# Performance work log

Hardware: AMD Instinct MI355X
Metric: run time of the kernel (lower is better)

## Reference

```python
import jax, jax.numpy as jnp
import numpy as np

NEG_SLOPE = 0.01  # torch leaky_relu default

def _lrelu(x):
    return jax.nn.leaky_relu(x, NEG_SLOPE)

def _l2norm(x, axis):
    # torch F.normalize(p=2, eps=1e-12)
    n = jnp.linalg.norm(x, axis=axis, keepdims=True)
    return x / jnp.maximum(n, 1e-12)

def setup_inputs() -> dict:
    key = jax.random.key(0)
    ks = jax.random.split(key, 12)
    Nda, Nq, C, Din, Dout = 10000, 64, 1024, 128, 256
    target_adj = (jax.random.uniform(ks[0], (Nda, Nda)) < 0.002).astype(jnp.float32)
    query_adj = (jax.random.uniform(ks[1], (Nq, Nq)) < 0.2).astype(jnp.float32)
    node_features_da = jax.random.normal(ks[2], (Nda, Din), dtype=jnp.float32)
    node_features_q = jax.random.normal(ks[3], (Nq, Din), dtype=jnp.float32)
    candidate_set = jax.random.randint(ks[4], (C,), 0, Nda)
    candidate_adj = (jax.random.uniform(ks[5], (C, C)) < 0.01).astype(jnp.float32)
    s_in = 1.0 / np.sqrt(Din).astype(np.float32)
    s_out = 1.0 / np.sqrt(Dout).astype(np.float32)
    W1_da = jax.random.normal(ks[6], (Din, Dout), dtype=jnp.float32) * s_in
    W1_q = jax.random.normal(ks[7], (Din, Dout), dtype=jnp.float32) * s_in
    W2_da = jax.random.normal(ks[8], (Dout, Dout), dtype=jnp.float32) * s_out
    W2_q = jax.random.normal(ks[9], (Dout, Dout), dtype=jnp.float32) * s_out
    threshold = jnp.float32(0.2)
    return {"target_adj": target_adj, "node_features_da": node_features_da,
            "query_adj": query_adj, "node_features_q": node_features_q,
            "candidate_set": candidate_set, "candidate_adj": candidate_adj,
            "threshold": threshold, "W1_da": W1_da, "W1_q": W1_q,
            "W2_da": W2_da, "W2_q": W2_q}

def _cross_cosine(q, da, candidate_set):
    # cosine similarity between each query node and each candidate target node: [Nq, C]
    return _l2norm(q, 1) @ _l2norm(da[candidate_set], 1).T

def reference(target_adj, node_features_da, query_adj, node_features_q,
              candidate_set, candidate_adj, threshold, W1_da, W1_q, W2_da, W2_q):
    # layer 1: GCN propagation on both graphs (gcn(adj,x) = adj @ x @ W)
    da1 = _lrelu(target_adj @ (node_features_da @ W1_da))   # [Nda, D]
    q1 = _lrelu(query_adj @ (node_features_q @ W1_q))       # [Nq, D]
    c1 = _cross_cosine(q1, da1, candidate_set)               # [Nq, C]
    pre_da1 = da1[candidate_set]                             # [C, D]
    # NOTE: da1[candidate_set].data = ... mutates a temporary in torch -> no-op on da1
    att_da1 = _lrelu(da1)                                    # dropout in eval = identity
    h1_q = c1 @ pre_da1                                      # [Nq, D]
    att_q1 = _lrelu(q1 + _l2norm(h1_q, 0))
    # layer 2
    da2 = _lrelu(target_adj @ (att_da1 @ W2_da))
    q2 = _lrelu(query_adj @ (att_q1 @ W2_q))
    c2 = _cross_cosine(q2, da2, candidate_set)
    pre_da2 = da2[candidate_set]
    att_da2 = _lrelu(da2)                                    # in-place update is again a no-op
    h2_q = c2 @ pre_da2
    att_q2 = _lrelu(q2 + _l2norm(h2_q, 0))
    # graph-level matching score per target node
    emb = jnp.mean(att_q2, axis=0, keepdims=True)            # [1, D]
    num = att_da2 @ emb[0]                                   # [Nda]
    den = jnp.maximum(jnp.linalg.norm(att_da2, axis=1) * jnp.linalg.norm(emb), 1e-8)
    end = (num / den)[None, :]                               # [1, Nda]
    # threshold selection expressed with a mask (jit-safe, same math: excluded
    # rows/cols are zero and do not affect L2 norms, sums, or the trace)
    m = (end[0] > threshold).astype(att_da2.dtype)           # [Nda]
    F_ = att_da2 * m[:, None]
    re_adj = F_ @ F_.T                                       # [Nda, Nda]
    nor_re = _l2norm(re_adj, 1) * target_adj                 # elementwise with original adj
    cnt = jnp.sum(m)
    total = jnp.sum(nor_re)
    tr = jnp.trace(nor_re)
    has = cnt > 0
    pre_avg_degree = jnp.where(has, total / jnp.maximum(cnt, 1.0), 0.0)
    pre_avg_nodes = jnp.where(has, tr, 0.0)
    pre_density = jnp.where(has, 2.0 * total / (tr * (tr - 1.0) + 1e-4), 0.0)
    return (end, att_da2, att_q2, pre_avg_degree, pre_density, pre_avg_nodes)
```

## Files before the change

kernel.cpp:

```cpp
#include <hip/hip_runtime.h>

constexpr int NDA = 10000;
constexpr int NQ  = 64;
constexpr int CND = 1024;
constexpr int DIN = 128;
constexpr int D   = 256;
constexpr int CAP = 96;

#define LRELU(x) ((x) >= 0.f ? (x) : 0.01f * (x))

__device__ __forceinline__ float wave_red64(float v) {
#pragma unroll
    for (int o = 32; o; o >>= 1) v += __shfl_down(v, o);
    return v;
}

__global__ __launch_bounds__(256) void build_csr(const float* __restrict__ adj,
                                                 int* __restrict__ cols,
                                                 int* __restrict__ rowcnt) {
    int row = blockIdx.x;
    __shared__ int scnt;
    if (threadIdx.x == 0) scnt = 0;
    __syncthreads();
    const float4* rp = (const float4*)(adj + (size_t)row * NDA);
    for (int i = threadIdx.x; i < NDA / 4; i += 256) {
        float4 v = rp[i];
        if (v.x != 0.f) { int s = atomicAdd(&scnt, 1); if (s < CAP) cols[row * CAP + s] = 4 * i; }
        if (v.y != 0.f) { int s = atomicAdd(&scnt, 1); if (s < CAP) cols[row * CAP + s] = 4 * i + 1; }
        if (v.z != 0.f) { int s = atomicAdd(&scnt, 1); if (s < CAP) cols[row * CAP + s] = 4 * i + 2; }
        if (v.w != 0.f) { int s = atomicAdd(&scnt, 1); if (s < CAP) cols[row * CAP + s] = 4 * i + 3; }
    }
    __syncthreads();
    if (threadIdx.x == 0) rowcnt[row] = min(scnt, CAP);
}

template <bool RELU_A, bool RELU_C>
__global__ __launch_bounds__(256) void gemm64(const float* __restrict__ A,
                                              const float* __restrict__ B,
                                              float* __restrict__ C,
                                              int M, int N, int K) {
    __shared__ float As[16][68];
    __shared__ float Bs[16][68];
    const int bm = blockIdx.x * 64;
    const int bn = blockIdx.y * 64;
    const int tid = threadIdx.x;
    const int tx = tid & 15, ty = tid >> 4;
    float acc[4][4] = {};
    for (int k0 = 0; k0 < K; k0 += 16) {
        {
            int m = tid >> 2;
            int k4 = (tid & 3) * 4;
            float4 v = make_float4(0.f, 0.f, 0.f, 0.f);
            if (bm + m < M) v = *(const float4*)(A + (size_t)(bm + m) * K + k0 + k4);
            if (RELU_A) { v.x = LRELU(v.x); v.y = LRELU(v.y); v.z = LRELU(v.z); v.w = LRELU(v.w); }
            As[k4 + 0][m] = v.x; As[k4 + 1][m] = v.y; As[k4 + 2][m] = v.z; As[k4 + 3][m] = v.w;
        }
        {
            int kk = tid >> 4;
            int n4 = (tid & 15) * 4;
            float4 v = *(const float4*)(B + (size_t)(k0 + kk) * N + bn + n4);
            Bs[kk][n4 + 0] = v.x; Bs[kk][n4 + 1] = v.y; Bs[kk][n4 + 2] = v.z; Bs[kk][n4 + 3] = v.w;
        }
        __syncthreads();
#pragma unroll
        for (int kk = 0; kk < 16; kk++) {
            float av[4], bv[4];
#pragma unroll
            for (int i = 0; i < 4; i++) av[i] = As[kk][ty * 4 + i];
#pragma unroll
            for (int j = 0; j < 4; j++) bv[j] = Bs[kk][tx * 4 + j];
#pragma unroll
            for (int i = 0; i < 4; i++)
#pragma unroll
                for (int j = 0; j < 4; j++) acc[i][j] += av[i] * bv[j];
        }
        __syncthreads();
    }
#pragma unroll
    for (int i = 0; i < 4; i++) {
        int r = bm + ty * 4 + i;
        if (r < M) {
            float4 v;
            v.x = acc[i][0]; v.y = acc[i][1]; v.z = acc[i][2]; v.w = acc[i][3];
            if (RELU_C) { v.x = LRELU(v.x); v.y = LRELU(v.y); v.z = LRELU(v.z); v.w = LRELU(v.w); }
            *(float4*)(C + (size_t)r * N + bn + tx * 4) = v;
        }
    }
}

__global__ __launch_bounds__(256) void spmm_csr(const int* __restrict__ cols,
                                                const int* __restrict__ rowcnt,
                                                const float* __restrict__ X,
                                                float* __restrict__ out1,
                                                float* __restrict__ out2) {
    int row = blockIdx.x;
    int d = threadIdx.x;
    int cnt = rowcnt[row];
    __shared__ int sc[CAP];
    if (d < cnt) sc[d] = cols[row * CAP + d];
    __syncthreads();
    float a0 = 0.f, a1 = 0.f, a2 = 0.f, a3 = 0.f;
    int k = 0;
    for (; k + 4 <= cnt; k += 4) {
        a0 += X[(size_t)sc[k + 0] * D + d];
        a1 += X[(size_t)sc[k + 1] * D + d];
        a2 += X[(size_t)sc[k + 2] * D + d];
        a3 += X[(size_t)sc[k + 3] * D + d];
    }
    for (; k < cnt; k++) a0 += X[(size_t)sc[k] * D + d];
    float v = LRELU(a0 + a1 + a2 + a3);
    out1[(size_t)row * D + d] = v;
    if (out2) out2[(size_t)row * D + d] = LRELU(v);
}

__global__ __launch_bounds__(256) void rownorms_kernel(const float* __restrict__ da,
                                                       const int* __restrict__ cand,
                                                       float* __restrict__ rnc,
                                                       const float* __restrict__ q,
                                                       float* __restrict__ rnq) {
    int b = blockIdx.x;
    const float* src;
    float* dst;
    if (b < CND) { src = da + (size_t)cand[b] * D; dst = rnc + b; }
    else         { src = q + (size_t)(b - CND) * D; dst = rnq + (b - CND); }
    float v = src[threadIdx.x];
    float p = wave_red64(v * v);
    __shared__ float red[4];
    int w = threadIdx.x >> 6, lane = threadIdx.x & 63;
    if (lane == 0) red[w] = p;
    __syncthreads();
    if (threadIdx.x == 0) *dst = sqrtf(red[0] + red[1] + red[2] + red[3]);
}

__global__ __launch_bounds__(256) void cosmat_kernel(const float* __restrict__ q,
                                                     const float* __restrict__ rnq,
                                                     const float* __restrict__ da,
                                                     const int* __restrict__ cand,
                                                     const float* __restrict__ rnc,
                                                     float* __restrict__ cm) {
    __shared__ float qs[D];
    int r = blockIdx.x;
    int cc = blockIdx.y * 256 + threadIdx.x;
    qs[threadIdx.x] = q[r * D + threadIdx.x];
    __syncthreads();
    int row = cand[cc];
    const float4* ap = (const float4*)(da + (size_t)row * D);
    float dot = 0.f;
#pragma unroll 8
    for (int k = 0; k < D / 4; k++) {
        float4 v = ap[k];
        dot += qs[4 * k] * v.x + qs[4 * k + 1] * v.y + qs[4 * k + 2] * v.z + qs[4 * k + 3] * v.w;
    }
    float denom = fmaxf(rnq[r], 1e-12f) * fmaxf(rnc[cc], 1e-12f);
    cm[r * CND + cc] = dot / denom;
}

__global__ __launch_bounds__(256) void hq_kernel(const float* __restrict__ cm,
                                                 const float* __restrict__ da,
                                                 const int* __restrict__ cand,
                                                 float* __restrict__ h) {
    __shared__ float swt[CND];
    __shared__ int sci[CND];
    int r = blockIdx.x, d = threadIdx.x;
    for (int s = 0; s < CND / 256; s++) {
        swt[s * 256 + d] = cm[r * CND + s * 256 + d];
        sci[s * 256 + d] = cand[s * 256 + d];
    }
    __syncthreads();
    float a0 = 0.f, a1 = 0.f, a2 = 0.f, a3 = 0.f, a4 = 0.f, a5 = 0.f, a6 = 0.f, a7 = 0.f;
    for (int c = 0; c < CND; c += 8) {
        a0 += swt[c + 0] * da[(size_t)sci[c + 0] * D + d];
        a1 += swt[c + 1] * da[(size_t)sci[c + 1] * D + d];
        a2 += swt[c + 2] * da[(size_t)sci[c + 2] * D + d];
        a3 += swt[c + 3] * da[(size_t)sci[c + 3] * D + d];
        a4 += swt[c + 4] * da[(size_t)sci[c + 4] * D + d];
        a5 += swt[c + 5] * da[(size_t)sci[c + 5] * D + d];
        a6 += swt[c + 6] * da[(size_t)sci[c + 6] * D + d];
        a7 += swt[c + 7] * da[(size_t)sci[c + 7] * D + d];
    }
    h[r * D + d] = ((a0 + a1) + (a2 + a3)) + ((a4 + a5) + (a6 + a7));
}

__global__ __launch_bounds__(256) void attq_kernel(const float* __restrict__ q,
                                                   const float* __restrict__ h,
                                                   float* __restrict__ attq,
                                                   float* __restrict__ emb) {
    int d = threadIdx.x;
    float hv[NQ];
    float ss = 0.f;
#pragma unroll
    for (int r = 0; r < NQ; r++) {
        hv[r] = h[r * D + d];
        ss += hv[r] * hv[r];
    }
    float inv = 1.f / fmaxf(sqrtf(ss), 1e-12f);
    float es = 0.f;
#pragma unroll
    for (int r = 0; r < NQ; r++) {
        float v = q[r * D + d] + hv[r] * inv;
        v = LRELU(v);
        attq[r * D + d] = v;
        es += v;
    }
    if (emb) {
        float e = es * (1.f / (float)NQ);
        emb[d] = e;
        float p = wave_red64(e * e);
        __shared__ float red[4];
        int w = d >> 6, lane = d & 63;
        if (lane == 0) red[w] = p;
        __syncthreads();
        if (d == 0) emb[D] = sqrtf(red[0] + red[1] + red[2] + red[3]);
    }
}

__global__ __launch_bounds__(256) void end_kernel(const float* __restrict__ A,
                                                  const float* __restrict__ emb,
                                                  const float* __restrict__ thr_p,
                                                  float* __restrict__ endv,
                                                  float* __restrict__ m,
                                                  float* __restrict__ cnt) {
    __shared__ float se[D];
    __shared__ float scnt;
    int d = threadIdx.x;
    se[d] = emb[d];
    if (d == 0) scnt = 0.f;
    __syncthreads();
    float embn = emb[D];
    float thr = *thr_p;
    int w = d >> 6, lane = d & 63;
    int row = blockIdx.x * 4 + w;
    const float* ar = A + (size_t)row * D;
    float num = 0.f, sq = 0.f;
#pragma unroll
    for (int s = 0; s < 4; s++) {
        float v = ar[lane + 64 * s];
        num += v * se[lane + 64 * s];
        sq += v * v;
    }
#pragma unroll
    for (int o = 32; o; o >>= 1) { num += __shfl_down(num, o); sq += __shfl_down(sq, o); }
    if (lane == 0) {
        float den = fmaxf(sqrtf(sq) * embn, 1e-8f);
        float e = num / den;
        endv[row] = e;
        float mv = e > thr ? 1.f : 0.f;
        m[row] = mv;
        if (mv != 0.f) atomicAdd(&scnt, 1.f);
    }
    __syncthreads();
    if (d == 0 && scnt != 0.f) atomicAdd(cnt, scnt);
}

constexpr int GCHUNK = 400;
__global__ __launch_bounds__(256) void G_kernel(const float* __restrict__ A,
                                                const float* __restrict__ m,
                                                float* __restrict__ G) {
    __shared__ float SA[8][64], SB[8][64];
    int ti = blockIdx.x >> 2, tj = blockIdx.x & 3;
    int base = blockIdx.y * GCHUNK;
    int tid = threadIdx.x;
    int tx = tid & 15, ty = tid >> 4;
    float acc[4][4] = {};
    for (int g0 = 0; g0 < GCHUNK; g0 += 8) {
        for (int l = tid; l < 512; l += 256) {
            int rr = l >> 6, c = l & 63;
            int r = base + g0 + rr;
            float mv = m[r];
            SA[rr][c] = A[(size_t)r * D + ti * 64 + c] * mv;
            SB[rr][c] = A[(size_t)r * D + tj * 64 + c];
        }
        __syncthreads();
#pragma unroll
        for (int rr = 0; rr < 8; rr++) {
            float av[4], bv[4];
#pragma unroll
            for (int i = 0; i < 4; i++) av[i] = SA[rr][ty * 4 + i];
#pragma unroll
            for (int j = 0; j < 4; j++) bv[j] = SB[rr][tx * 4 + j];
#pragma unroll
            for (int i = 0; i < 4; i++)
#pragma unroll
                for (int j = 0; j < 4; j++) acc[i][j] += av[i] * bv[j];
        }
        __syncthreads();
    }
#pragma unroll
    for (int i = 0; i < 4; i++)
#pragma unroll
        for (int j = 0; j < 4; j++)
            atomicAdd(&G[(ti * 64 + ty * 4 + i) * D + tj * 64 + tx * 4 + j], acc[i][j]);
}

__global__ __launch_bounds__(256) void final_kernel(const int* __restrict__ cols,
                                                    const int* __restrict__ rowcnt,
                                                    const float* __restrict__ m,
                                                    const float* __restrict__ A,
                                                    const float* __restrict__ H,
                                                    double* __restrict__ total,
                                                    double* __restrict__ tr) {
    int i = blockIdx.x;
    if (m[i] == 0.f) return;
    __shared__ float sa[D];
    __shared__ int sc[CAP];
    __shared__ float red[4], red2[4];
    __shared__ float sdenom;
    int d = threadIdx.x;
    float av = A[(size_t)i * D + d];
    sa[d] = av;
    int cnt = rowcnt[i];
    if (d < cnt) sc[d] = cols[i * CAP + d];
    float p = wave_red64(av * H[(size_t)i * D + d]);
    int w = d >> 6, lane = d & 63;
    if (lane == 0) red[w] = p;
    __syncthreads();
    if (d == 0) sdenom = fmaxf(sqrtf(red[0] + red[1] + red[2] + red[3]), 1e-12f);
    __syncthreads();
    float accs = 0.f, acct = 0.f;
    for (int k = w; k < cnt; k += 4) {
        int j = sc[k];
        if (m[j] != 0.f) {
            const float* aj = A + (size_t)j * D;
            float t = sa[lane] * aj[lane] + sa[lane + 64] * aj[lane + 64]
                    + sa[lane + 128] * aj[lane + 128] + sa[lane + 192] * aj[lane + 192];
            t = wave_red64(t);
            if (lane == 0) { accs += t; if (j == i) acct += t; }
        }
    }
    if (lane == 0) { red[w] = accs; red2[w] = acct; }
    __syncthreads();
    if (d == 0) {
        float s = red[0] + red[1] + red[2] + red[3];
        float t2 = red2[0] + red2[1] + red2[2] + red2[3];
        double inv = 1.0 / (double)sdenom;
        if (s != 0.f) atomicAdd(total, (double)s * inv);
        if (t2 != 0.f) atomicAdd(tr, (double)t2 * inv);
    }
}

__global__ void scalars_kernel(const float* __restrict__ cnt,
                               const double* __restrict__ total,
                               const double* __restrict__ tr,
                               float* __restrict__ out) {
    float c = *cnt;
    float T = (float)*total;
    float R = (float)*tr;
    bool has = c > 0.f;
    out[0] = has ? (T / fmaxf(c, 1.f)) : 0.f;
    out[1] = has ? (2.f * T / (R * (R - 1.f) + 1e-4f)) : 0.f;
    out[2] = has ? R : 0.f;
}

extern "C" void kernel_launch(void* const* d_in, const int* in_sizes, int n_in,
                              void* d_out, int out_size, void* d_ws, size_t ws_size,
                              hipStream_t stream) {
    (void)in_sizes; (void)n_in; (void)out_size; (void)ws_size;
    const float* adj  = (const float*)d_in[0];
    const float* Fda  = (const float*)d_in[1];
    const float* Qadj = (const float*)d_in[2];
    const float* Fq   = (const float*)d_in[3];
    const int*   cand = (const int*)d_in[4];
    const float* thr  = (const float*)d_in[6];
    const float* W1da = (const float*)d_in[7];
    const float* W1q  = (const float*)d_in[8];
    const float* W2da = (const float*)d_in[9];
    const float* W2q  = (const float*)d_in[10];

    float* out = (float*)d_out;
    float* o_end    = out;
    float* o_attda2 = out + NDA;
    float* o_attq2  = out + NDA + (size_t)NDA * D;
    float* o_sc     = o_attq2 + NQ * D;

    char* w = (char*)d_ws;
    size_t off = 0;
    auto alloc = [&](size_t b) { size_t r = off; off += (b + 255) & ~(size_t)255; return r; };
    float* bufA = (float*)(w + alloc((size_t)NDA * D * 4));
    float* bufB = (float*)(w + alloc((size_t)NDA * D * 4));
    float* bufC = (float*)(w + alloc((size_t)NDA * D * 4));
    int* colsb   = (int*)(w + alloc((size_t)NDA * CAP * 4));
    int* rowcntb = (int*)(w + alloc((size_t)NDA * 4));
    float* mbuf  = (float*)(w + alloc((size_t)NDA * 4));
    char* zbase = w + alloc(262144 + 256);
    float* Gb    = (float*)zbase;
    float* cntb  = (float*)(zbase + 262144);
    double* totb = (double*)(zbase + 262144 + 8);
    double* trb  = (double*)(zbase + 262144 + 16);
    float* xq   = (float*)(w + alloc((size_t)NQ * D * 4));
    float* q1b  = (float*)(w + alloc((size_t)NQ * D * 4));
    float* aq1  = (float*)(w + alloc((size_t)NQ * D * 4));
    float* q2b  = (float*)(w + alloc((size_t)NQ * D * 4));
    float* hb   = (float*)(w + alloc((size_t)NQ * D * 4));
    float* cm   = (float*)(w + alloc((size_t)NQ * CND * 4));
    float* rnc  = (float*)(w + alloc((size_t)CND * 4));
    float* rnq  = (float*)(w + alloc((size_t)NQ * 4));
    float* embb = (float*)(w + alloc((size_t)(D + 1) * 4));

    hipMemsetAsync(zbase, 0, 262144 + 256, stream);

    const dim3 gBig((NDA + 63) / 64, D / 64);
    const dim3 gSmall(1, D / 64);

    gemm64<false, false><<<gBig, 256, 0, stream>>>(Fda, W1da, bufA, NDA, D, DIN);
    build_csr<<<NDA, 256, 0, stream>>>(adj, colsb, rowcntb);
    gemm64<false, false><<<gSmall, 256, 0, stream>>>(Fq, W1q, xq, NQ, D, DIN);
    gemm64<false, true><<<gSmall, 256, 0, stream>>>(Qadj, xq, q1b, NQ, D, NQ);
    spmm_csr<<<NDA, 256, 0, stream>>>(colsb, rowcntb, bufA, bufB, (float*)nullptr);
    rownorms_kernel<<<CND + NQ, 256, 0, stream>>>(bufB, cand, rnc, q1b, rnq);
    cosmat_kernel<<<dim3(NQ, CND / 256), 256, 0, stream>>>(q1b, rnq, bufB, cand, rnc, cm);
    hq_kernel<<<NQ, 256, 0, stream>>>(cm, bufB, cand, hb);
    attq_kernel<<<1, 256, 0, stream>>>(q1b, hb, aq1, (float*)nullptr);
    gemm64<true, false><<<gBig, 256, 0, stream>>>(bufB, W2da, bufA, NDA, D, D);
    gemm64<false, false><<<gSmall, 256, 0, stream>>>(aq1, W2q, xq, NQ, D, D);
    gemm64<false, true><<<gSmall, 256, 0, stream>>>(Qadj, xq, q2b, NQ, D, NQ);
    spmm_csr<<<NDA, 256, 0, stream>>>(colsb, rowcntb, bufA, bufC, o_attda2);
    rownorms_kernel<<<CND + NQ, 256, 0, stream>>>(bufC, cand, rnc, q2b, rnq);
    cosmat_kernel<<<dim3(NQ, CND / 256), 256, 0, stream>>>(q2b, rnq, bufC, cand, rnc, cm);
    hq_kernel<<<NQ, 256, 0, stream>>>(cm, bufC, cand, hb);
    attq_kernel<<<1, 256, 0, stream>>>(q2b, hb, o_attq2, embb);
    end_kernel<<<NDA / 4, 256, 0, stream>>>(o_attda2, embb, thr, o_end, mbuf, cntb);
    G_kernel<<<dim3(16, NDA / GCHUNK), 256, 0, stream>>>(o_attda2, mbuf, Gb);
    gemm64<false, false><<<gBig, 256, 0, stream>>>(o_attda2, Gb, bufB, NDA, D, D);
    final_kernel<<<NDA, 256, 0, stream>>>(colsb, rowcntb, mbuf, o_attda2, bufB, totb, trb);
    scalars_kernel<<<1, 1, 0, stream>>>(cntb, totb, trb, o_sc);
}
```

Measured before the change: 1.027 ms.

## Reassociate GCN layers, fuse query path, and compute cross-attention via candidate Gram matrix

Layer 1 now aggregates the 128-wide input features over the sparse adjacency before multiplying by W1, and layer 2 likewise aggregates the activated features before the W2 GEMM, so the SpMM gathers narrower or equal rows and the leaky ReLU moves into the GEMM epilogue. The query-side X@W and adj@X are fused into one qpath kernel. The cosine-matrix-then-weighted-gather path is replaced by a 256x256 candidate Gram matrix M built once, followed by a small q@M GEMM, which avoids the random gathers in hq_kernel. The leaky ReLU placement changes (activation now applied after the dense GEMM rather than after aggregation), and it needs careful checking that it still matches the reference semantics.

```diff
diff --git a/kernel.cpp b/kernel.cpp
--- a/kernel.cpp
+++ b/kernel.cpp
@@ -34,10 +34,40 @@
     if (threadIdx.x == 0) rowcnt[row] = min(scnt, CAP);
 }
 
-template <bool RELU_A, bool RELU_C>
+template <int W, bool RELU_IN>
+__global__ void spmm(const int* __restrict__ cols,
+                     const int* __restrict__ rowcnt,
+                     const float* __restrict__ X,
+                     float* __restrict__ out) {
+    int row = blockIdx.x;
+    int d = threadIdx.x;
+    int cnt = rowcnt[row];
+    __shared__ int sc[CAP];
+    if (d < CAP && d < cnt) sc[d] = cols[row * CAP + d];
+    __syncthreads();
+    float a0 = 0.f, a1 = 0.f, a2 = 0.f, a3 = 0.f;
+    int k = 0;
+    for (; k + 4 <= cnt; k += 4) {
+        float v0 = X[(size_t)sc[k + 0] * W + d];
+        float v1 = X[(size_t)sc[k + 1] * W + d];
+        float v2 = X[(size_t)sc[k + 2] * W + d];
+        float v3 = X[(size_t)sc[k + 3] * W + d];
+        if (RELU_IN) { v0 = LRELU(v0); v1 = LRELU(v1); v2 = LRELU(v2); v3 = LRELU(v3); }
+        a0 += v0; a1 += v1; a2 += v2; a3 += v3;
+    }
+    for (; k < cnt; k++) {
+        float v = X[(size_t)sc[k] * W + d];
+        if (RELU_IN) v = LRELU(v);
+        a0 += v;
+    }
+    out[(size_t)row * W + d] = (a0 + a1) + (a2 + a3);
+}
+
+template <bool RELU_C, bool DUAL>
 __global__ __launch_bounds__(256) void gemm64(const float* __restrict__ A,
                                               const float* __restrict__ B,
                                               float* __restrict__ C,
+                                              float* __restrict__ C2,
                                               int M, int N, int K) {
     __shared__ float As[16][68];
     __shared__ float Bs[16][68];
@@ -52,7 +82,6 @@
             int k4 = (tid & 3) * 4;
             float4 v = make_float4(0.f, 0.f, 0.f, 0.f);
             if (bm + m < M) v = *(const float4*)(A + (size_t)(bm + m) * K + k0 + k4);
-            if (RELU_A) { v.x = LRELU(v.x); v.y = LRELU(v.y); v.z = LRELU(v.z); v.w = LRELU(v.w); }
             As[k4 + 0][m] = v.x; As[k4 + 1][m] = v.y; As[k4 + 2][m] = v.z; As[k4 + 3][m] = v.w;
         }
         {
@@ -84,101 +113,185 @@
             v.x = acc[i][0]; v.y = acc[i][1]; v.z = acc[i][2]; v.w = acc[i][3];
             if (RELU_C) { v.x = LRELU(v.x); v.y = LRELU(v.y); v.z = LRELU(v.z); v.w = LRELU(v.w); }
             *(float4*)(C + (size_t)r * N + bn + tx * 4) = v;
-        }
-    }
-}
-
-__global__ __launch_bounds__(256) void spmm_csr(const int* __restrict__ cols,
-                                                const int* __restrict__ rowcnt,
-                                                const float* __restrict__ X,
-                                                float* __restrict__ out1,
-                                                float* __restrict__ out2) {
-    int row = blockIdx.x;
-    int d = threadIdx.x;
-    int cnt = rowcnt[row];
-    __shared__ int sc[CAP];
-    if (d < cnt) sc[d] = cols[row * CAP + d];
-    __syncthreads();
-    float a0 = 0.f, a1 = 0.f, a2 = 0.f, a3 = 0.f;
-    int k = 0;
-    for (; k + 4 <= cnt; k += 4) {
-        a0 += X[(size_t)sc[k + 0] * D + d];
-        a1 += X[(size_t)sc[k + 1] * D + d];
-        a2 += X[(size_t)sc[k + 2] * D + d];
-        a3 += X[(size_t)sc[k + 3] * D + d];
-    }
-    for (; k < cnt; k++) a0 += X[(size_t)sc[k] * D + d];
-    float v = LRELU(a0 + a1 + a2 + a3);
-    out1[(size_t)row * D + d] = v;
-    if (out2) out2[(size_t)row * D + d] = LRELU(v);
+            if (DUAL) {
+                float4 u;
+                u.x = LRELU(v.x); u.y = LRELU(v.y); u.z = LRELU(v.z); u.w = LRELU(v.w);
+                *(float4*)(C2 + (size_t)r * N + bn + tx * 4) = u;
+            }
+        }
+    }
+}
+
+__global__ __launch_bounds__(256) void qpath_kernel(const float* __restrict__ Fq,
+                                                    const float* __restrict__ Wq,
+                                                    const float* __restrict__ Qadj,
+                                                    float* __restrict__ q_out,
+                                                    int K) {
+    __shared__ float As[16][68];
+    __shared__ float Bs[16][68];
+    __shared__ float Xs[64][68];
+    __shared__ float Qs[64][68];
+    const int bn = blockIdx.x * 64;
+    const int tid = threadIdx.x;
+    const int tx = tid & 15, ty = tid >> 4;
+    float acc[4][4] = {};
+    for (int k0 = 0; k0 < K; k0 += 16) {
+        {
+            int m = tid >> 2;
+            int k4 = (tid & 3) * 4;
+            float4 v = *(const float4*)(Fq + (size_t)m * K + k0 + k4);
+            As[k4 + 0][m] = v.x; As[k4 + 1][m] = v.y; As[k4 + 2][m] = v.z; As[k4 + 3][m] = v.w;
+        }
+        {
+            int kk = tid >> 4;
+            int n4 = (tid & 15) * 4;
+            float4 v = *(const float4*)(Wq + (size_t)(k0 + kk) * D + bn + n4);
+            Bs[kk][n4 + 0] = v.x; Bs[kk][n4 + 1] = v.y; Bs[kk][n4 + 2] = v.z; Bs[kk][n4 + 3] = v.w;
+        }
+        __syncthreads();
+#pragma unroll
+        for (int kk = 0; kk < 16; kk++) {
+            float av[4], bv[4];
+#pragma unroll
+            for (int i = 0; i < 4; i++) av[i] = As[kk][ty * 4 + i];
+#pragma unroll
+            for (int j = 0; j < 4; j++) bv[j] = Bs[kk][tx * 4 + j];
+#pragma unroll
+            for (int i = 0; i < 4; i++)
+#pragma unroll
+                for (int j = 0; j < 4; j++) acc[i][j] += av[i] * bv[j];
+        }
+        __syncthreads();
+    }
+#pragma unroll
+    for (int i = 0; i < 4; i++)
+#pragma unroll
+        for (int j = 0; j < 4; j++) Xs[ty * 4 + i][tx * 4 + j] = acc[i][j];
+    for (int l = tid; l < NQ * NQ; l += 256) Qs[l >> 6][l & 63] = Qadj[l];
+    __syncthreads();
+    float a2[4][4] = {};
+#pragma unroll 4
+    for (int kk = 0; kk < NQ; kk++) {
+        float av[4], bv[4];
+#pragma unroll
+        for (int i = 0; i < 4; i++) av[i] = Qs[ty * 4 + i][kk];
+#pragma unroll
+        for (int j = 0; j < 4; j++) bv[j] = Xs[kk][tx * 4 + j];
+#pragma unroll
+        for (int i = 0; i < 4; i++)
+#pragma unroll
+            for (int j = 0; j < 4; j++) a2[i][j] += av[i] * bv[j];
+    }
+#pragma unroll
+    for (int i = 0; i < 4; i++)
+#pragma unroll
+        for (int j = 0; j < 4; j++)
+            q_out[(ty * 4 + i) * D + bn + tx * 4 + j] = LRELU(a2[i][j]);
 }
 
 __global__ __launch_bounds__(256) void rownorms_kernel(const float* __restrict__ da,
                                                        const int* __restrict__ cand,
-                                                       float* __restrict__ rnc,
+                                                       float* __restrict__ rncinv,
                                                        const float* __restrict__ q,
-                                                       float* __restrict__ rnq) {
+                                                       float* __restrict__ rnqinv) {
     int b = blockIdx.x;
     const float* src;
     float* dst;
-    if (b < CND) { src = da + (size_t)cand[b] * D; dst = rnc + b; }
-    else         { src = q + (size_t)(b - CND) * D; dst = rnq + (b - CND); }
+    if (b < CND) { src = da + (size_t)cand[b] * D; dst = rncinv + b; }
+    else         { src = q + (size_t)(b - CND) * D; dst = rnqinv + (b - CND); }
     float v = src[threadIdx.x];
     float p = wave_red64(v * v);
     __shared__ float red[4];
     int w = threadIdx.x >> 6, lane = threadIdx.x & 63;
     if (lane == 0) red[w] = p;
     __syncthreads();
-    if (threadIdx.x == 0) *dst = sqrtf(red[0] + red[1] + red[2] + red[3]);
-}
-
-__global__ __launch_bounds__(256) void cosmat_kernel(const float* __restrict__ q,
-                                                     const float* __restrict__ rnq,
-                                                     const float* __restrict__ da,
-                                                     const int* __restrict__ cand,
-                                                     const float* __restrict__ rnc,
-                                                     float* __restrict__ cm) {
-    __shared__ float qs[D];
-    int r = blockIdx.x;
-    int cc = blockIdx.y * 256 + threadIdx.x;
-    qs[threadIdx.x] = q[r * D + threadIdx.x];
-    __syncthreads();
-    int row = cand[cc];
-    const float4* ap = (const float4*)(da + (size_t)row * D);
-    float dot = 0.f;
-#pragma unroll 8
-    for (int k = 0; k < D / 4; k++) {
-        float4 v = ap[k];
-        dot += qs[4 * k] * v.x + qs[4 * k + 1] * v.y + qs[4 * k + 2] * v.z + qs[4 * k + 3] * v.w;
-    }
-    float denom = fmaxf(rnq[r], 1e-12f) * fmaxf(rnc[cc], 1e-12f);
-    cm[r * CND + cc] = dot / denom;
-}
-
-__global__ __launch_bounds__(256) void hq_kernel(const float* __restrict__ cm,
-                                                 const float* __restrict__ da,
-                                                 const int* __restrict__ cand,
-                                                 float* __restrict__ h) {
-    __shared__ float swt[CND];
-    __shared__ int sci[CND];
-    int r = blockIdx.x, d = threadIdx.x;
-    for (int s = 0; s < CND / 256; s++) {
-        swt[s * 256 + d] = cm[r * CND + s * 256 + d];
-        sci[s * 256 + d] = cand[s * 256 + d];
-    }
-    __syncthreads();
-    float a0 = 0.f, a1 = 0.f, a2 = 0.f, a3 = 0.f, a4 = 0.f, a5 = 0.f, a6 = 0.f, a7 = 0.f;
-    for (int c = 0; c < CND; c += 8) {
-        a0 += swt[c + 0] * da[(size_t)sci[c + 0] * D + d];
-        a1 += swt[c + 1] * da[(size_t)sci[c + 1] * D + d];
-        a2 += swt[c + 2] * da[(size_t)sci[c + 2] * D + d];
-        a3 += swt[c + 3] * da[(size_t)sci[c + 3] * D + d];
-        a4 += swt[c + 4] * da[(size_t)sci[c + 4] * D + d];
-        a5 += swt[c + 5] * da[(size_t)sci[c + 5] * D + d];
-        a6 += swt[c + 6] * da[(size_t)sci[c + 6] * D + d];
-        a7 += swt[c + 7] * da[(size_t)sci[c + 7] * D + d];
-    }
-    h[r * D + d] = ((a0 + a1) + (a2 + a3)) + ((a4 + a5) + (a6 + a7));
+    if (threadIdx.x == 0) *dst = 1.f / fmaxf(sqrtf(red[0] + red[1] + red[2] + red[3]), 1e-12f);
+}
+
+__global__ __launch_bounds__(256) void candM_kernel(const float* __restrict__ da,
+                                                    const int* __restrict__ cand,
+                                                    const float* __restrict__ rncinv,
+                                                    float* __restrict__ M) {
+    __shared__ float SA[8][64], SB[8][64];
+    const int ti = blockIdx.x, tj = blockIdx.y;
+    const int tid = threadIdx.x;
+    const int tx = tid & 15, ty = tid >> 4;
+    float acc[4][4] = {};
+    for (int c0 = 0; c0 < CND; c0 += 8) {
+        for (int l = tid; l < 512; l += 256) {
+            int rr = l >> 6, c = l & 63;
+            int cr = cand[c0 + rr];
+            float s = rncinv[c0 + rr];
+            SA[rr][c] = da[(size_t)cr * D + ti * 64 + c] * s;
+            SB[rr][c] = da[(size_t)cr * D + tj * 64 + c];
+        }
+        __syncthreads();
+#pragma unroll
+        for (int rr = 0; rr < 8; rr++) {
+            float av[4], bv[4];
+#pragma unroll
+            for (int i = 0; i < 4; i++) av[i] = SA[rr][ty * 4 + i];
+#pragma unroll
+            for (int j = 0; j < 4; j++) bv[j] = SB[rr][tx * 4 + j];
+#pragma unroll
+            for (int i = 0; i < 4; i++)
+#pragma unroll
+                for (int j = 0; j < 4; j++) acc[i][j] += av[i] * bv[j];
+        }
+        __syncthreads();
+    }
+#pragma unroll
+    for (int i = 0; i < 4; i++)
+#pragma unroll
+        for (int j = 0; j < 4; j++)
+            M[(ti * 64 + ty * 4 + i) * D + tj * 64 + tx * 4 + j] = acc[i][j];
+}
+
+__global__ __launch_bounds__(256) void hq_gemm(const float* __restrict__ q,
+                                               const float* __restrict__ rnqinv,
+                                               const float* __restrict__ M,
+                                               float* __restrict__ h) {
+    __shared__ float As[16][68];
+    __shared__ float Bs[16][68];
+    const int bn = blockIdx.x * 64;
+    const int tid = threadIdx.x;
+    const int tx = tid & 15, ty = tid >> 4;
+    float acc[4][4] = {};
+    for (int k0 = 0; k0 < D; k0 += 16) {
+        {
+            int m = tid >> 2;
+            int k4 = (tid & 3) * 4;
+            float s = rnqinv[m];
+            float4 v = *(const float4*)(q + (size_t)m * D + k0 + k4);
+            As[k4 + 0][m] = v.x * s; As[k4 + 1][m] = v.y * s;
+            As[k4 + 2][m] = v.z * s; As[k4 + 3][m] = v.w * s;
+        }
+        {
+            int kk = tid >> 4;
+            int n4 = (tid & 15) * 4;
+            float4 v = *(const float4*)(M + (size_t)(k0 + kk) * D + bn + n4);
+            Bs[kk][n4 + 0] = v.x; Bs[kk][n4 + 1] = v.y; Bs[kk][n4 + 2] = v.z; Bs[kk][n4 + 3] = v.w;
+        }
+        __syncthreads();
+#pragma unroll
+        for (int kk = 0; kk < 16; kk++) {
+            float av[4], bv[4];
+#pragma unroll
+            for (int i = 0; i < 4; i++) av[i] = As[kk][ty * 4 + i];
+#pragma unroll
+            for (int j = 0; j < 4; j++) bv[j] = Bs[kk][tx * 4 + j];
+#pragma unroll
+            for (int i = 0; i < 4; i++)
+#pragma unroll
+                for (int j = 0; j < 4; j++) acc[i][j] += av[i] * bv[j];
+        }
+        __syncthreads();
+    }
+#pragma unroll
+    for (int i = 0; i < 4; i++)
+#pragma unroll
+        for (int j = 0; j < 4; j++)
+            h[(ty * 4 + i) * D + bn + tx * 4 + j] = acc[i][j];
 }
 
 __global__ __launch_bounds__(256) void attq_kernel(const float* __restrict__ q,
@@ -386,41 +499,37 @@
     float* cntb  = (float*)(zbase + 262144);
     double* totb = (double*)(zbase + 262144 + 8);
     double* trb  = (double*)(zbase + 262144 + 16);
-    float* xq   = (float*)(w + alloc((size_t)NQ * D * 4));
     float* q1b  = (float*)(w + alloc((size_t)NQ * D * 4));
     float* aq1  = (float*)(w + alloc((size_t)NQ * D * 4));
     float* q2b  = (float*)(w + alloc((size_t)NQ * D * 4));
     float* hb   = (float*)(w + alloc((size_t)NQ * D * 4));
-    float* cm   = (float*)(w + alloc((size_t)NQ * CND * 4));
-    float* rnc  = (float*)(w + alloc((size_t)CND * 4));
-    float* rnq  = (float*)(w + alloc((size_t)NQ * 4));
-    float* embb = (float*)(w + alloc((size_t)(D + 1) * 4));
+    float* Mb   = (float*)(w + alloc((size_t)D * D * 4));
+    float* rncinv = (float*)(w + alloc((size_t)CND * 4));
+    float* rnqinv = (float*)(w + alloc((size_t)NQ * 4));
+    float* embb   = (float*)(w + alloc((size_t)(D + 1) * 4));
 
     hipMemsetAsync(zbase, 0, 262144 + 256, stream);
 
     const dim3 gBig((NDA + 63) / 64, D / 64);
-    const dim3 gSmall(1, D / 64);
-
-    gemm64<false, false><<<gBig, 256, 0, stream>>>(Fda, W1da, bufA, NDA, D, DIN);
+
     build_csr<<<NDA, 256, 0, stream>>>(adj, colsb, rowcntb);
-    gemm64<false, false><<<gSmall, 256, 0, stream>>>(Fq, W1q, xq, NQ, D, DIN);
-    gemm64<false, true><<<gSmall, 256, 0, stream>>>(Qadj, xq, q1b, NQ, D, NQ);
-    spmm_csr<<<NDA, 256, 0, stream>>>(colsb, rowcntb, bufA, bufB, (float*)nullptr);
-    rownorms_kernel<<<CND + NQ, 256, 0, stream>>>(bufB, cand, rnc, q1b, rnq);
-    cosmat_kernel<<<dim3(NQ, CND / 256), 256, 0, stream>>>(q1b, rnq, bufB, cand, rnc, cm);
-    hq_kernel<<<NQ, 256, 0, stream>>>(cm, bufB, cand, hb);
-    attq_kernel<<<1, 256, 0, stream>>>(q1b, hb, aq1, (float*)nullptr);
-    gemm64<true, false><<<gBig, 256, 0, stream>>>(bufB, W2da, bufA, NDA, D, D);
-    gemm64<false, false><<<gSmall, 256, 0, stream>>>(aq1, W2q, xq, NQ, D, D);
-    gemm64<false, true><<<gSmall, 256, 0, stream>>>(Qadj, xq, q2b, NQ, D, NQ);
-    spmm_csr<<<NDA, 256, 0, stream>>>(colsb, rowcntb, bufA, bufC, o_attda2);
-    rownorms_kernel<<<CND + NQ, 256, 0, stream>>>(bufC, cand, rnc, q2b, rnq);
-    cosmat_kernel<<<dim3(NQ, CND / 256), 256, 0, stream>>>(q2b, rnq, bufC, cand, rnc, cm);
-    hq_kernel<<<NQ, 256, 0, stream>>>(cm, bufC, cand, hb);
+    qpath_kernel<<<D / 64, 256, 0, stream>>>(Fq, W1q, Qadj, q1b, DIN);
+    spmm<DIN, false><<<NDA, DIN, 0, stream>>>(colsb, rowcntb, Fda, bufA);
+    gemm64<true, false><<<gBig, 256, 0, stream>>>(bufA, W1da, bufB, nullptr, NDA, D, DIN);
+    rownorms_kernel<<<CND + NQ, 256, 0, stream>>>(bufB, cand, rncinv, q1b, rnqinv);
+    candM_kernel<<<dim3(4, 4), 256, 0, stream>>>(bufB, cand, rncinv, Mb);
+    hq_gemm<<<D / 64, 256, 0, stream>>>(q1b, rnqinv, Mb, hb);
+    attq_kernel<<<1, 256, 0, stream>>>(q1b, hb, aq1, nullptr);
+    qpath_kernel<<<D / 64, 256, 0, stream>>>(aq1, W2q, Qadj, q2b, D);
+    spmm<D, true><<<NDA, D, 0, stream>>>(colsb, rowcntb, bufB, bufA);
+    gemm64<true, true><<<gBig, 256, 0, stream>>>(bufA, W2da, bufC, o_attda2, NDA, D, D);
+    rownorms_kernel<<<CND + NQ, 256, 0, stream>>>(bufC, cand, rncinv, q2b, rnqinv);
+    candM_kernel<<<dim3(4, 4), 256, 0, stream>>>(bufC, cand, rncinv, Mb);
+    hq_gemm<<<D / 64, 256, 0, stream>>>(q2b, rnqinv, Mb, hb);
     attq_kernel<<<1, 256, 0, stream>>>(q2b, hb, o_attq2, embb);
     end_kernel<<<NDA / 4, 256, 0, stream>>>(o_attda2, embb, thr, o_end, mbuf, cntb);
     G_kernel<<<dim3(16, NDA / GCHUNK), 256, 0, stream>>>(o_attda2, mbuf, Gb);
-    gemm64<false, false><<<gBig, 256, 0, stream>>>(o_attda2, Gb, bufB, NDA, D, D);
+    gemm64<false, false><<<gBig, 256, 0, stream>>>(o_attda2, Gb, bufB, nullptr, NDA, D, D);
     final_kernel<<<NDA, 256, 0, stream>>>(colsb, rowcntb, mbuf, o_attda2, bufB, totb, trb);
     scalars_kernel<<<1, 1, 0, stream>>>(cntb, totb, trb, o_sc);
 }
```

Measured after the change: 1.252 ms. 21.9% more time.
